# Optimization experiments

Hardware: AMD Instinct MI355X
Metric: run time of the kernel (lower is better)

The kernel has to match this reference:

```python
import jax, jax.numpy as jnp
import numpy as np


def compute_intervals(samples, L):
    """Build per-node [lower, upper) intervals for a complete binary tree.
    samples: (dim, 2^L - 1) betas, node j's beta splits its interval.
    Returns lowers, uppers: (dim, 2^L - 1), nodes in breadth-first order.
    Mirrors Tree.get_intervals: left child = [lo, lo + b*len],
    right child = [lo + b*len, lo + b*len + (1-b)*len].
    """
    dim = samples.shape[0]
    lo = jnp.zeros((dim, 1), samples.dtype)
    hi = jnp.ones((dim, 1), samples.dtype)
    lows, his = [lo], [hi]
    for l in range(L - 1):
        b = samples[:, 2**l - 1: 2**(l + 1) - 1]  # betas of level-l nodes (dim, 2^l)
        length = hi - lo
        split = lo + b * length
        right_hi = split + (1.0 - b) * length
        # children of node n are 2n+1 (left), 2n+2 (right) -> interleave
        lo = jnp.stack([lo, split], axis=-1).reshape(dim, -1)
        hi = jnp.stack([split, right_hi], axis=-1).reshape(dim, -1)
        lows.append(lo)
        his.append(hi)
    return jnp.concatenate(lows, axis=1), jnp.concatenate(his, axis=1)


def setup_inputs() -> dict:
    key = jax.random.key(0)
    k1, k2 = jax.random.split(key)
    n, dim, L = 1000000, 16, 8
    # points strictly inside (0,1) so the root interval (0,1] contains all of them
    x = jax.random.uniform(k1, (n, dim), jnp.float32, 1e-4, 1.0 - 1e-4)
    # sampled betas (stand-in for Beta(shapes,scales).rsample()), bounded away from 0/1
    samples = jax.random.uniform(k2, (dim, 2**L - 1), jnp.float32, 0.05, 0.95)
    return {"x": x, "samples": samples, "L": L}


def reference(x, samples, L):
    n, dim = x.shape
    lowers, uppers = compute_intervals(samples, L)  # (dim, n_nodes)
    loT, hiT, bT = lowers.T, uppers.T, samples.T    # (n_nodes, dim)
    d = jnp.arange(dim)[None, :]                    # (1, dim)
    idx = jnp.zeros((n, dim), jnp.int32)            # current node per (point, dim)
    log_y = jnp.zeros((n, dim), x.dtype)
    # Tree descent replaces the original's dense (n, dim, 2^L-1) containment
    # mask + nonzero + retry loop; the path visits exactly L nodes per (point, dim).
    for l in range(L):
        b = bT[idx, d]                              # (n, dim) beta at current node
        log_y = log_y + jnp.log(b)                  # prod of betas along path (in log)
        if l < L - 1:
            lo = loT[idx, d]
            hi = hiT[idx, d]
            split = lo + b * (hi - lo)
            # original containment: lower < x <= upper, so x <= split -> left child
            idx = jnp.where(x <= split, 2 * idx + 1, 2 * idx + 2)
    leaf_len = hiT[idx, d] - loT[idx, d]            # B at the leaf node
    return (log_y - jnp.log(leaf_len)).mean(axis=-1)  # (n,)
```

## Files before the change

### kernel.cpp

```cpp
#include <hip/hip_runtime.h>
#include <math.h>


constexpr int DIMS     = 16;
constexpr int NODES    = 255;
constexpr int INTERNAL = 127;

__global__ __launch_bounds__(256) void polya_fused(
    const float* __restrict__ x,
    const float* __restrict__ samples,
    float* __restrict__ out,
    int n)
{
#pragma clang fp contract(off)
    __shared__ float s_split[DIMS * 128];
    __shared__ float s_value[DIMS * 128];

    {
        const int lane = threadIdx.x & 63;
        const int wid  = threadIdx.x >> 6;
#pragma unroll
        for (int dd = 0; dd < 4; ++dd) {
            const int d = wid * 4 + dd;
            const float* s = samples + d * NODES;
            float lo = 0.0f, hi = 1.0f, ac = 0.0f;
            float sp = 0.0f, rhi = 0.0f, ac2 = 0.0f;
#pragma unroll
            for (int l = 0; l <= 6; ++l) {
                if (l > 0) {
                    const int pl = lane >> 1;
                    const float plo = __shfl(lo,  pl);
                    const float psp = __shfl(sp,  pl);
                    const float prh = __shfl(rhi, pl);
                    const float pac = __shfl(ac2, pl);
                    lo = (lane & 1) ? psp : plo;
                    hi = (lane & 1) ? prh : psp;
                    ac = pac;
                }
                if (lane < (1 << l)) {
                    const int i = (1 << l) - 1 + lane;
                    const float b = s[i];
                    const float len = hi - lo;
                    sp  = lo + b * len;
                    rhi = sp + (1.0f - b) * len;
                    ac2 = ac + logf(b);
                    s_split[(d << 7) + i] = sp;
                    if (l == 6) {
                        const int jl = 2 * i + 1;
                        const float vl = ac2 + logf(s[jl])     - logf(sp  - lo);
                        const float vr = ac2 + logf(s[jl + 1]) - logf(rhi - sp);
                        s_value[(d << 7) + 2 * lane]     = vl;
                        s_value[(d << 7) + 2 * lane + 1] = vr;
                    }
                }
            }
        }
    }
    __syncthreads();

    const int stride = gridDim.x * 256;
    for (int p = blockIdx.x * 256 + threadIdx.x; p < n; p += stride) {
        const float4* xr = reinterpret_cast<const float4*>(x + (size_t)p * DIMS);
        float4 a = xr[0], b4 = xr[1], c4 = xr[2], e4 = xr[3];
        float xv[DIMS] = {a.x, a.y, a.z, a.w,  b4.x, b4.y, b4.z, b4.w,
                          c4.x, c4.y, c4.z, c4.w,  e4.x, e4.y, e4.z, e4.w};
        int   q[DIMS];
        float sp[DIMS];
#pragma unroll
        for (int d = 0; d < DIMS; ++d) q[d] = 0;
#pragma unroll
        for (int l = 0; l < 7; ++l) {
#pragma unroll
            for (int d = 0; d < DIMS; ++d)
                sp[d] = s_split[(d << 7) + q[d]];
#pragma unroll
            for (int d = 0; d < DIMS; ++d)
                q[d] = 2 * q[d] + 1 + (int)(xv[d] > sp[d]);
        }
        float acc = 0.0f;
#pragma unroll
        for (int d = 0; d < DIMS; ++d)
            acc += s_value[(d << 7) + (q[d] - INTERNAL)];
        out[p] = acc * 0.0625f;
    }
}

extern "C" void kernel_launch(void* const* d_in, const int* in_sizes, int n_in,
                              void* d_out, int out_size, void* d_ws, size_t ws_size,
                              hipStream_t stream) {
    const float* x       = (const float*)d_in[0];
    const float* samples = (const float*)d_in[1];
    float* out = (float*)d_out;
    const int n = in_sizes[0] / DIMS;

    int blocks = (n + 255) / 256;
    if (blocks > 1024) blocks = 1024;
    polya_fused<<<blocks, 256, 0, stream>>>(x, samples, out, n);
}
```

Measured before the change: 35.45 us.

## Map one thread per (point, dim) with DPP row reduction and padded LDS

Changes the work decomposition so each thread handles a single (point, dimension) element instead of a whole 16-dim point. Global reads of x become fully coalesced scalar loads, and the 16 per-dim leaf values are summed with DPP row-rotate adds inside each 16-lane row. The LDS tables are padded to a stride of 129 to reduce bank conflicts, since lanes now index different dimension rows at once. The grid is fixed at 2048 blocks. In exchange, only one lane in 16 writes output and the reduction adds cross-lane ops per point.

```diff
diff --git a/kernel.cpp b/kernel.cpp
--- a/kernel.cpp
+++ b/kernel.cpp
@@ -2,9 +2,16 @@
 #include <math.h>
 
 
-constexpr int DIMS     = 16;
-constexpr int NODES    = 255;
-constexpr int INTERNAL = 127;
+constexpr int DIMS    = 16;
+constexpr int NODES   = 255;
+constexpr int STRIDE  = 129;
+constexpr int LDSW    = DIMS * STRIDE;
+
+template <int N>
+__device__ __forceinline__ float row_ror_addf(float f) {
+    int r = __builtin_amdgcn_update_dpp(0, __float_as_int(f), 0x120 + N, 0xF, 0xF, true);
+    return f + __int_as_float(r);
+}
 
 __global__ __launch_bounds__(256) void polya_fused(
     const float* __restrict__ x,
@@ -13,8 +20,8 @@
     int n)
 {
 #pragma clang fp contract(off)
-    __shared__ float s_split[DIMS * 128];
-    __shared__ float s_value[DIMS * 128];
+    __shared__ float s_split[LDSW];
+    __shared__ float s_value[LDSW];
 
     {
         const int lane = threadIdx.x & 63;
@@ -44,13 +51,13 @@
                     sp  = lo + b * len;
                     rhi = sp + (1.0f - b) * len;
                     ac2 = ac + logf(b);
-                    s_split[(d << 7) + i] = sp;
+                    s_split[d * STRIDE + i] = sp;
                     if (l == 6) {
                         const int jl = 2 * i + 1;
                         const float vl = ac2 + logf(s[jl])     - logf(sp  - lo);
                         const float vr = ac2 + logf(s[jl + 1]) - logf(rhi - sp);
-                        s_value[(d << 7) + 2 * lane]     = vl;
-                        s_value[(d << 7) + 2 * lane + 1] = vr;
+                        s_value[d * STRIDE + 2 * lane]     = vl;
+                        s_value[d * STRIDE + 2 * lane + 1] = vr;
                     }
                 }
             }
@@ -58,30 +65,26 @@
     }
     __syncthreads();
 
-    const int stride = gridDim.x * 256;
-    for (int p = blockIdx.x * 256 + threadIdx.x; p < n; p += stride) {
-        const float4* xr = reinterpret_cast<const float4*>(x + (size_t)p * DIMS);
-        float4 a = xr[0], b4 = xr[1], c4 = xr[2], e4 = xr[3];
-        float xv[DIMS] = {a.x, a.y, a.z, a.w,  b4.x, b4.y, b4.z, b4.w,
-                          c4.x, c4.y, c4.z, c4.w,  e4.x, e4.y, e4.z, e4.w};
-        int   q[DIMS];
-        float sp[DIMS];
-#pragma unroll
-        for (int d = 0; d < DIMS; ++d) q[d] = 0;
+    const unsigned total   = (unsigned)n * 16u;
+    const unsigned gstride = gridDim.x * 256u;
+    const unsigned gid     = blockIdx.x * 256u + threadIdx.x;
+    const int dbase = (int)(gid & 15u) * STRIDE;
+    const bool writer = (gid & 15u) == 0u;
+
+    for (unsigned w = gid; w < total; w += gstride) {
+        const float xv = x[w];
+        int q = 0;
 #pragma unroll
         for (int l = 0; l < 7; ++l) {
-#pragma unroll
-            for (int d = 0; d < DIMS; ++d)
-                sp[d] = s_split[(d << 7) + q[d]];
-#pragma unroll
-            for (int d = 0; d < DIMS; ++d)
-                q[d] = 2 * q[d] + 1 + (int)(xv[d] > sp[d]);
+            const float sp = s_split[dbase + q];
+            q = 2 * q + 1 + (int)(xv > sp);
         }
-        float acc = 0.0f;
-#pragma unroll
-        for (int d = 0; d < DIMS; ++d)
-            acc += s_value[(d << 7) + (q[d] - INTERNAL)];
-        out[p] = acc * 0.0625f;
+        float f = s_value[dbase + (q - 127)];
+        f = row_ror_addf<1>(f);
+        f = row_ror_addf<2>(f);
+        f = row_ror_addf<4>(f);
+        f = row_ror_addf<8>(f);
+        if (writer) out[w >> 4] = f * 0.0625f;
     }
 }
 
@@ -93,7 +96,5 @@
     float* out = (float*)d_out;
     const int n = in_sizes[0] / DIMS;
 
-    int blocks = (n + 255) / 256;
-    if (blocks > 1024) blocks = 1024;
-    polya_fused<<<blocks, 256, 0, stream>>>(x, samples, out, n);
+    polya_fused<<<2048, 256, 0, stream>>>(x, samples, out, n);
 }
```

Measured after the change: 44.96 us. +26.8%, slower.

## Process two points per thread with non-persistent grid and waves-per-EU hint

Applied to the files above, without the earlier changes.

Replaces the persistent grid-stride loop (capped at 1024 blocks) with a one-shot grid where each thread handles two points, issuing both points' loads up front. The descent loop is reordered to iterate per dimension, interleaving two independent LDS lookup chains. An amdgpu_waves_per_eu(6) attribute asks the compiler to limit registers for occupancy. In exchange, every block now rebuilds the shared-memory tables, about 1950 blocks instead of 1024, which adds setup overhead per block.

```diff
diff --git a/kernel.cpp b/kernel.cpp
--- a/kernel.cpp
+++ b/kernel.cpp
@@ -2,11 +2,11 @@
 #include <math.h>
 
 
-constexpr int DIMS     = 16;
-constexpr int NODES    = 255;
-constexpr int INTERNAL = 127;
+constexpr int DIMS  = 16;
+constexpr int NODES = 255;
 
-__global__ __launch_bounds__(256) void polya_fused(
+__global__ __launch_bounds__(256) __attribute__((amdgpu_waves_per_eu(6)))
+void polya_fused(
     const float* __restrict__ x,
     const float* __restrict__ samples,
     float* __restrict__ out,
@@ -58,31 +58,37 @@
     }
     __syncthreads();
 
-    const int stride = gridDim.x * 256;
-    for (int p = blockIdx.x * 256 + threadIdx.x; p < n; p += stride) {
-        const float4* xr = reinterpret_cast<const float4*>(x + (size_t)p * DIMS);
-        float4 a = xr[0], b4 = xr[1], c4 = xr[2], e4 = xr[3];
-        float xv[DIMS] = {a.x, a.y, a.z, a.w,  b4.x, b4.y, b4.z, b4.w,
-                          c4.x, c4.y, c4.z, c4.w,  e4.x, e4.y, e4.z, e4.w};
-        int   q[DIMS];
-        float sp[DIMS];
+    const int p0 = blockIdx.x * 512 + threadIdx.x;
+    const int p1 = p0 + 256;
+    const int lp0 = (p0 < n) ? p0 : 0;
+    const int lp1 = (p1 < n) ? p1 : 0;
+
+    const float4* xr0 = reinterpret_cast<const float4*>(x + (size_t)lp0 * DIMS);
+    const float4* xr1 = reinterpret_cast<const float4*>(x + (size_t)lp1 * DIMS);
+    float4 a0 = xr0[0], b0v = xr0[1], c0 = xr0[2], e0 = xr0[3];
+    float4 a1 = xr1[0], b1v = xr1[1], c1 = xr1[2], e1 = xr1[3];
+    float xa[DIMS] = {a0.x, a0.y, a0.z, a0.w,  b0v.x, b0v.y, b0v.z, b0v.w,
+                      c0.x, c0.y, c0.z, c0.w,  e0.x,  e0.y,  e0.z,  e0.w};
+    float xb[DIMS] = {a1.x, a1.y, a1.z, a1.w,  b1v.x, b1v.y, b1v.z, b1v.w,
+                      c1.x, c1.y, c1.z, c1.w,  e1.x,  e1.y,  e1.z,  e1.w};
+
+    float acc0 = 0.0f, acc1 = 0.0f;
 #pragma unroll
-        for (int d = 0; d < DIMS; ++d) q[d] = 0;
+    for (int d = 0; d < DIMS; ++d) {
+        const float xv0 = xa[d], xv1 = xb[d];
+        int q0 = 0, q1 = 0;
 #pragma unroll
         for (int l = 0; l < 7; ++l) {
-#pragma unroll
-            for (int d = 0; d < DIMS; ++d)
-                sp[d] = s_split[(d << 7) + q[d]];
-#pragma unroll
-            for (int d = 0; d < DIMS; ++d)
-                q[d] = 2 * q[d] + 1 + (int)(xv[d] > sp[d]);
+            const float sp0 = s_split[(d << 7) + q0];
+            const float sp1 = s_split[(d << 7) + q1];
+            q0 = 2 * q0 + 1 + (int)(xv0 > sp0);
+            q1 = 2 * q1 + 1 + (int)(xv1 > sp1);
         }
-        float acc = 0.0f;
-#pragma unroll
-        for (int d = 0; d < DIMS; ++d)
-            acc += s_value[(d << 7) + (q[d] - INTERNAL)];
-        out[p] = acc * 0.0625f;
+        acc0 += s_value[(d << 7) + (q0 - 127)];
+        acc1 += s_value[(d << 7) + (q1 - 127)];
     }
+    if (p0 < n) out[p0] = acc0 * 0.0625f;
+    if (p1 < n) out[p1] = acc1 * 0.0625f;
 }
 
 extern "C" void kernel_launch(void* const* d_in, const int* in_sizes, int n_in,
@@ -93,7 +99,6 @@
     float* out = (float*)d_out;
     const int n = in_sizes[0] / DIMS;
 
-    int blocks = (n + 255) / 256;
-    if (blocks > 1024) blocks = 1024;
+    const int blocks = (n + 511) / 512;
     polya_fused<<<blocks, 256, 0, stream>>>(x, samples, out, n);
 }
```

New measurement: 34.77 us. No clear change (-1.9%).
